# Performance work log

Hardware: AMD Instinct MI355X
Metric: run time of the kernel (lower is better)

The kernel has to match this reference:

```python
import jax, jax.numpy as jnp
import numpy as np

B, P, D_IN = 128, 4096, 4   # frames, points/frame, xyz+time
NG = 16                      # number of trajectory groups
H1, H2, H3 = 64, 128, 512    # PointNet shared-MLP widths


def _init_mlp(key, dims):
    ks = jax.random.split(key, len(dims) - 1)
    params = []
    for k, (di, do) in zip(ks, zip(dims[:-1], dims[1:])):
        W = jax.random.normal(k, (di, do), dtype=jnp.float32) * (1.0 / np.sqrt(di))
        b = jnp.zeros((do,), dtype=jnp.float32)
        params.append((W, b))
    return params


def setup_inputs() -> dict:
    key = jax.random.key(0)
    k_pc, k_t, k_idx, k_g, k_l = jax.random.split(key, 5)
    pc = jax.random.normal(k_pc, (B, 3, P), dtype=jnp.float32)
    traj_time_batch = jax.random.uniform(k_t, (B, 1), dtype=jnp.float32)
    traj_inbatch_index = jnp.sort(jax.random.randint(k_idx, (B,), 0, NG)).astype(jnp.int32)
    (Wg1, bg1), (Wg2, bg2), (Wg3, bg3) = _init_mlp(k_g, [D_IN, H1, H2, H3])
    (Wl1, bl1), (Wl2, bl2), (Wl3, bl3) = _init_mlp(k_l, [D_IN, H1, H2, H3])
    return dict(pc=pc, traj_time_batch=traj_time_batch, traj_inbatch_index=traj_inbatch_index,
                Wg1=Wg1, bg1=bg1, Wg2=Wg2, bg2=bg2, Wg3=Wg3, bg3=bg3,
                Wl1=Wl1, bl1=bl1, Wl2=Wl2, bl2=bl2, Wl3=Wl3, bl3=bl3)


def _mlp(x, layers):
    # pointwise shared MLP: x [..., P, d_in] -> [..., P, d_out]
    for W, b in layers:
        x = jax.nn.relu(x @ W + b)
    return x


def reference(pc, traj_time_batch, traj_inbatch_index,
              Wg1, bg1, Wg2, bg2, Wg3, bg3,
              Wl1, bl1, Wl2, bl2, Wl3, bl3):
    b, _, p = pc.shape
    # append time channel: [B,3,P] + [B,1,P] -> [B,4,P]
    t = jnp.broadcast_to(traj_time_batch[..., None], (b, 1, p))
    feat = jnp.concatenate([pc, t], axis=1)
    x = jnp.swapaxes(feat, 1, 2)  # [B,P,4] points-last layout for pointwise MLP

    # global branch: shared MLP on every point, then max over all points of each trajectory group
    hg = _mlp(x, [(Wg1, bg1), (Wg2, bg2), (Wg3, bg3)])           # [B,P,H3]
    seg = jnp.repeat(traj_inbatch_index, p)                       # [B*P]
    gmax = jax.ops.segment_max(hg.reshape(b * p, -1), seg, num_segments=NG)  # [NG,H3]
    global_feat = gmax[traj_inbatch_index]                        # [B,H3] broadcast back per frame

    # local branch: per-frame PointNet encode (shared MLP + max over points)
    hl = _mlp(x, [(Wl1, bl1), (Wl2, bl2), (Wl3, bl3)])            # [B,P,H3]
    local_feat = hl.max(axis=1)                                   # [B,H3]

    z = jnp.concatenate([global_feat, local_feat], axis=1)        # [B,2*H3]
    input_features_vis = pc                                       # original pc (last dim == 4096, no slice)
    return (z, input_features_vis)
```

## Files before the change

kernel.cpp:

```cpp
#include <hip/hip_runtime.h>
#include <hip/hip_bf16.h>

#define NB   128
#define NP   4096
#define NGRP 16
#define C3   512

typedef __bf16 bf16x8 __attribute__((ext_vector_type(8)));
typedef __bf16 bf16x4 __attribute__((ext_vector_type(4)));
typedef float  f32x4  __attribute__((ext_vector_type(4)));

#define WS_W1F_G 0
#define WS_W1F_L 4096
#define WS_W2F_G 8192
#define WS_W2F_L 24576
#define WS_W3F_G 40960
#define WS_W3F_L 172032
#define WS_GMAX  303104

__global__ __launch_bounds__(256) void prep_kernel(
    const float* __restrict__ Wg1, const float* __restrict__ Wg2, const float* __restrict__ Wg3,
    const float* __restrict__ Wl1, const float* __restrict__ Wl2, const float* __restrict__ Wl3,
    float* __restrict__ out, char* __restrict__ ws) {
    const int t = blockIdx.x, tid = threadIdx.x;
    if (t >= 37) {
        #pragma unroll
        for (int j = 0; j < 8; ++j) out[(t - 37) * 2048 + j * 256 + tid] = 0.0f;
        return;
    }
    if (t == 36) {
        float* gmax = (float*)(ws + WS_GMAX);
        #pragma unroll
        for (int k = 0; k < 32; ++k) gmax[k * 256 + tid] = 0.0f;
        int c = tid >> 6, lane = tid & 63;
        int ch = c * 16 + (lane & 15);
        int kb = (lane >> 4) * 8;
        bf16x8 pg, pl;
        #pragma unroll
        for (int j = 0; j < 8; ++j) {
            int k = kb + j;
            pg[j] = (k < 4) ? (__bf16)Wg1[k * 64 + ch] : (__bf16)0.0f;
            pl[j] = (k < 4) ? (__bf16)Wl1[k * 64 + ch] : (__bf16)0.0f;
        }
        *(bf16x8*)((__bf16*)(ws + WS_W1F_G) + c * 512 + lane * 8) = pg;
        *(bf16x8*)((__bf16*)(ws + WS_W1F_L) + c * 512 + lane * 8) = pl;
        return;
    }
    __shared__ float tile[64][65];
    const float* src; __bf16* dst; int cBase, mMul, srcStride;
    if (t < 32) {
        int branch = t >> 4, rem = t & 15;
        int tk = rem >> 3, tc = rem & 7;
        src = (branch ? Wl3 : Wg3) + (size_t)(tk * 64) * 512 + tc * 64;
        dst = (__bf16*)(ws + (branch ? WS_W3F_L : WS_W3F_G));
        cBase = tc * 16 + tk * 2; mMul = 4; srcStride = 512;
    } else {
        int u = t - 32; int branch = u >> 1, tc = u & 1;
        src = (branch ? Wl2 : Wg2) + tc * 64;
        dst = (__bf16*)(ws + (branch ? WS_W2F_L : WS_W2F_G));
        cBase = tc * 8; mMul = 2; srcStride = 128;
    }
    {
        int r0 = tid >> 6, cl = tid & 63;
        #pragma unroll
        for (int p = 0; p < 16; ++p)
            tile[p * 4 + r0][cl] = src[(size_t)(p * 4 + r0) * srcStride + cl];
    }
    __syncthreads();
    int lane = tid & 63, l15 = lane & 15, q = lane >> 4;
    #pragma unroll
    for (int cc = 0; cc < 2; ++cc) {
        int pair = (tid >> 6) * 2 + cc;
        int mi = pair >> 1, ks = pair & 1;
        bf16x8 pk;
        #pragma unroll
        for (int j = 0; j < 8; ++j) pk[j] = (__bf16)tile[ks * 32 + q * 8 + j][mi * 16 + l15];
        *(bf16x8*)(dst + (cBase + mi * mMul + ks) * 512 + lane * 8) = pk;
    }
}

__global__ __launch_bounds__(512, 2) void main_kernel(
    const float* __restrict__ pc, const float* __restrict__ tt, const int* __restrict__ idx,
    const float* __restrict__ bg1, const float* __restrict__ bg2, const float* __restrict__ bg3,
    const float* __restrict__ bl1, const float* __restrict__ bl2, const float* __restrict__ bl3,
    float* __restrict__ out, char* __restrict__ ws) {
    __shared__ __align__(16) char smem[41728];
    __bf16* h2f = (__bf16*)smem;
    __bf16* h1f = (__bf16*)(smem + 32768);
    float*  b1s = (float*)(smem + 40960);
    float*  b2s = (float*)(smem + 41216);

    const int tid = threadIdx.x, lane = tid & 63, wave = tid >> 6;
    const int quad = lane >> 4, l15 = lane & 15;
    const int branch = blockIdx.y;
    const int frame = blockIdx.x >> 2, p0 = (blockIdx.x & 3) * 1024;

    const float* pcx = pc + (size_t)frame * 3 * NP;

    if (branch == 0) {
        f32x4* pd = (f32x4*)(out + NB * 2 * C3 + (size_t)frame * 3 * NP + p0);
        const f32x4* ps = (const f32x4*)(pcx + p0);
        for (int i = tid; i < 768; i += 512) {
            int r = i >> 8, col = i & 255;
            pd[r * (NP / 4) + col] = ps[r * (NP / 4) + col];
        }
    }

    const __bf16* w1g = (const __bf16*)(ws + (branch ? WS_W1F_L : WS_W1F_G));
    const __bf16* w2g = (const __bf16*)(ws + (branch ? WS_W2F_L : WS_W2F_G));
    const __bf16* w3g = (const __bf16*)(ws + (branch ? WS_W3F_L : WS_W3F_G));
    const float* b1 = branch ? bl1 : bg1;
    const float* b2 = branch ? bl2 : bg2;
    const float* b3 = branch ? bl3 : bg3;

    if (tid < 64)  b1s[tid] = b1[tid];
    if (tid < 128) b2s[tid] = b2[tid];

    bf16x8 a1[4];
    #pragma unroll
    for (int mi = 0; mi < 4; ++mi) a1[mi] = *(const bf16x8*)(w1g + mi * 512 + lane * 8);
    bf16x8 a2[2];
    #pragma unroll
    for (int ks = 0; ks < 2; ++ks)
        a2[ks] = *(const bf16x8*)(w2g + (wave * 2 + ks) * 512 + lane * 8);
    bf16x8 aw[4][4];
    #pragma unroll
    for (int mi = 0; mi < 4; ++mi)
        #pragma unroll
        for (int ks = 0; ks < 4; ++ks)
            aw[mi][ks] = *(const bf16x8*)(w3g + ((wave * 4 + mi) * 4 + ks) * 512 + lane * 8);

    const float tval = tt[frame];
    const f32x4 zf = {0.0f, 0.0f, 0.0f, 0.0f};
    f32x4 runmax[4];
    #pragma unroll
    for (int mi = 0; mi < 4; ++mi) runmax[mi] = (f32x4){-1e30f, -1e30f, -1e30f, -1e30f};

    const bool l1wave = (wave < 4);
    const int pw = (wave & 3) * 16 + l15;
    const int kq2 = (wave * 2 + (quad >> 1)) & 3;
    const int s2  = wave >> 1;

    auto do_l1 = [&](float xx, float xy, float xz) {
        bf16x8 xb;
        #pragma unroll
        for (int j = 0; j < 8; ++j) xb[j] = (__bf16)0.0f;
        if (quad == 0) { xb[0] = (__bf16)xx; xb[1] = (__bf16)xy; xb[2] = (__bf16)xz; xb[3] = (__bf16)tval; }
        #pragma unroll
        for (int mi = 0; mi < 4; ++mi) {
            f32x4 c = __builtin_amdgcn_mfma_f32_16x16x32_bf16(a1[mi], xb, zf, 0, 0, 0);
            f32x4 bv = *(const f32x4*)(b1s + mi * 16 + quad * 4);
            bf16x4 pk;
            #pragma unroll
            for (int r = 0; r < 4; ++r) pk[r] = (__bf16)fmaxf(c[r] + bv[r], 0.0f);
            const int kq = (mi & 1) * 2 + (quad >> 1);
            *(bf16x4*)(h1f + ((wave & 3) * 2 + (mi >> 1)) * 512 + kq * 128 + l15 * 8 + (quad & 1) * 4) = pk;
        }
    };
    auto do_l2 = [&](__bf16* hbn) {
        #pragma unroll
        for (int ni = 0; ni < 4; ++ni) {
            bf16x8 q0 = *(const bf16x8*)(h1f + (ni * 2 + 0) * 512 + lane * 8);
            bf16x8 q1 = *(const bf16x8*)(h1f + (ni * 2 + 1) * 512 + lane * 8);
            f32x4 c = __builtin_amdgcn_mfma_f32_16x16x32_bf16(a2[0], q0, zf, 0, 0, 0);
            c = __builtin_amdgcn_mfma_f32_16x16x32_bf16(a2[1], q1, c, 0, 0, 0);
            f32x4 bv = *(const f32x4*)(b2s + wave * 16 + quad * 4);
            bf16x4 pk;
            #pragma unroll
            for (int r = 0; r < 4; ++r) pk[r] = (__bf16)fmaxf(c[r] + bv[r], 0.0f);
            *(bf16x4*)(hbn + (ni * 4 + s2) * 512 + kq2 * 128 + l15 * 8 + (quad & 1) * 4) = pk;
        }
    };
    auto p2_group = [&](const __bf16* hb, int ni) {
        bf16x8 bh[4];
        #pragma unroll
        for (int ks = 0; ks < 4; ++ks)
            bh[ks] = *(const bf16x8*)(hb + (ni * 4 + ks) * 512 + lane * 8);
        f32x4 acc[4];
        #pragma unroll
        for (int ks = 0; ks < 4; ++ks)
            #pragma unroll
            for (int mi = 0; mi < 4; ++mi)
                acc[mi] = __builtin_amdgcn_mfma_f32_16x16x32_bf16(
                    aw[mi][ks], bh[ks], ks ? acc[mi] : zf, 0, 0, 0);
        #pragma unroll
        for (int mi = 0; mi < 4; ++mi)
            #pragma unroll
            for (int r = 0; r < 4; ++r)
                runmax[mi][r] = fmaxf(runmax[mi][r], acc[mi][r]);
    };

    __syncthreads();

    if (l1wave) {
        float xx = pcx[p0 + pw], xy = pcx[NP + p0 + pw], xz = pcx[2 * NP + p0 + pw];
        do_l1(xx, xy, xz);
    }
    __syncthreads();
    do_l2(h2f);

    for (int m = 0; m < 16; ++m) {
        __syncthreads();
        const __bf16* hb = h2f + (m & 1) * 8192;
        __bf16* hbn = h2f + ((m + 1) & 1) * 8192;
        const bool more = (m < 15);
        float nx = 0.f, ny = 0.f, nz = 0.f;
        if (more && l1wave) {
            const int p = p0 + (m + 1) * 64 + pw;
            nx = pcx[p]; ny = pcx[NP + p]; nz = pcx[2 * NP + p];
        }
        p2_group(hb, 0);
        p2_group(hb, 1);
        if (more && l1wave) do_l1(nx, ny, nz);
        __syncthreads();
        p2_group(hb, 2);
        p2_group(hb, 3);
        if (more) do_l2(hbn);
    }

    const int g = idx[frame];
    float* gmax = (float*)(ws + WS_GMAX);
    unsigned* dst = (branch == 0) ? (unsigned*)(gmax + g * C3)
                                  : (unsigned*)(out + (size_t)frame * (2 * C3) + C3);
    #pragma unroll
    for (int mi = 0; mi < 4; ++mi) {
        f32x4 v = runmax[mi];
        #pragma unroll
        for (int d = 1; d < 16; d <<= 1) {
            #pragma unroll
            for (int r = 0; r < 4; ++r) v[r] = fmaxf(v[r], __shfl_xor(v[r], d));
        }
        if (l15 == 0) {
            #pragma unroll
            for (int r = 0; r < 4; ++r) {
                const int ch = wave * 64 + mi * 16 + quad * 4 + r;
                const float fv = fmaxf(v[r] + b3[ch], 0.0f);
                atomicMax(dst + ch, __float_as_uint(fv));
            }
        }
    }
}

__global__ void gather_kernel(const int* __restrict__ idx, const char* __restrict__ ws,
                              float* __restrict__ out) {
    int i = blockIdx.x * blockDim.x + threadIdx.x;
    int b = i >> 9, ch = i & 511;
    const float* gmax = (const float*)(ws + WS_GMAX);
    out[b * (2 * C3) + ch] = gmax[idx[b] * C3 + ch];
}

extern "C" void kernel_launch(void* const* d_in, const int* in_sizes, int n_in,
                              void* d_out, int out_size, void* d_ws, size_t ws_size,
                              hipStream_t stream) {
    const float* pc  = (const float*)d_in[0];
    const float* tt  = (const float*)d_in[1];
    const int*   idx = (const int*)d_in[2];
    const float* Wg1 = (const float*)d_in[3];  const float* bg1 = (const float*)d_in[4];
    const float* Wg2 = (const float*)d_in[5];  const float* bg2 = (const float*)d_in[6];
    const float* Wg3 = (const float*)d_in[7];  const float* bg3 = (const float*)d_in[8];
    const float* Wl1 = (const float*)d_in[9];  const float* bl1 = (const float*)d_in[10];
    const float* Wl2 = (const float*)d_in[11]; const float* bl2 = (const float*)d_in[12];
    const float* Wl3 = (const float*)d_in[13]; const float* bl3 = (const float*)d_in[14];
    float* out = (float*)d_out;
    char*  ws  = (char*)d_ws;

    prep_kernel<<<101, 256, 0, stream>>>(Wg1, Wg2, Wg3, Wl1, Wl2, Wl3, out, ws);
    main_kernel<<<dim3(512, 2), 512, 0, stream>>>(pc, tt, idx, bg1, bg2, bg3,
                                                  bl1, bl2, bl3, out, ws);
    gather_kernel<<<256, 256, 0, stream>>>(idx, ws, out);
}
```

Measured before the change: 226.4 us.

## Fuse weight prep and gather into a warp-specialized per-frame kernel

Launches one block per frame and branch, splitting the waves into producers and consumers. Four producer waves compute layers 1 and 2 into double-buffered shared memory, while four consumer waves run the layer-3 MFMAs and a running max over 512 channels. The separate weight-prep and gather kernels are removed: weights are converted to bf16 fragments straight from fp32 global memory, and a last-arriving-block counter does the per-group max and broadcast. This drops launch overhead and the atomics, but only half the waves do the dominant layer-3 work, there are 4x fewer blocks, and 128 registers of weight fragments plus 32 of running max under the (512, 2) launch bounds risks register spills.

```diff
diff --git a/kernel.cpp b/kernel.cpp
--- a/kernel.cpp
+++ b/kernel.cpp
@@ -3,112 +3,48 @@
 
 #define NB   128
 #define NP   4096
-#define NGRP 16
 #define C3   512
 
 typedef __bf16 bf16x8 __attribute__((ext_vector_type(8)));
 typedef __bf16 bf16x4 __attribute__((ext_vector_type(4)));
 typedef float  f32x4  __attribute__((ext_vector_type(4)));
 
-#define WS_W1F_G 0
-#define WS_W1F_L 4096
-#define WS_W2F_G 8192
-#define WS_W2F_L 24576
-#define WS_W3F_G 40960
-#define WS_W3F_L 172032
-#define WS_GMAX  303104
-
-__global__ __launch_bounds__(256) void prep_kernel(
-    const float* __restrict__ Wg1, const float* __restrict__ Wg2, const float* __restrict__ Wg3,
-    const float* __restrict__ Wl1, const float* __restrict__ Wl2, const float* __restrict__ Wl3,
-    float* __restrict__ out, char* __restrict__ ws) {
-    const int t = blockIdx.x, tid = threadIdx.x;
-    if (t >= 37) {
-        #pragma unroll
-        for (int j = 0; j < 8; ++j) out[(t - 37) * 2048 + j * 256 + tid] = 0.0f;
-        return;
-    }
-    if (t == 36) {
-        float* gmax = (float*)(ws + WS_GMAX);
-        #pragma unroll
-        for (int k = 0; k < 32; ++k) gmax[k * 256 + tid] = 0.0f;
-        int c = tid >> 6, lane = tid & 63;
-        int ch = c * 16 + (lane & 15);
-        int kb = (lane >> 4) * 8;
-        bf16x8 pg, pl;
-        #pragma unroll
-        for (int j = 0; j < 8; ++j) {
-            int k = kb + j;
-            pg[j] = (k < 4) ? (__bf16)Wg1[k * 64 + ch] : (__bf16)0.0f;
-            pl[j] = (k < 4) ? (__bf16)Wl1[k * 64 + ch] : (__bf16)0.0f;
-        }
-        *(bf16x8*)((__bf16*)(ws + WS_W1F_G) + c * 512 + lane * 8) = pg;
-        *(bf16x8*)((__bf16*)(ws + WS_W1F_L) + c * 512 + lane * 8) = pl;
-        return;
-    }
-    __shared__ float tile[64][65];
-    const float* src; __bf16* dst; int cBase, mMul, srcStride;
-    if (t < 32) {
-        int branch = t >> 4, rem = t & 15;
-        int tk = rem >> 3, tc = rem & 7;
-        src = (branch ? Wl3 : Wg3) + (size_t)(tk * 64) * 512 + tc * 64;
-        dst = (__bf16*)(ws + (branch ? WS_W3F_L : WS_W3F_G));
-        cBase = tc * 16 + tk * 2; mMul = 4; srcStride = 512;
-    } else {
-        int u = t - 32; int branch = u >> 1, tc = u & 1;
-        src = (branch ? Wl2 : Wg2) + tc * 64;
-        dst = (__bf16*)(ws + (branch ? WS_W2F_L : WS_W2F_G));
-        cBase = tc * 8; mMul = 2; srcStride = 128;
-    }
-    {
-        int r0 = tid >> 6, cl = tid & 63;
-        #pragma unroll
-        for (int p = 0; p < 16; ++p)
-            tile[p * 4 + r0][cl] = src[(size_t)(p * 4 + r0) * srcStride + cl];
-    }
-    __syncthreads();
-    int lane = tid & 63, l15 = lane & 15, q = lane >> 4;
-    #pragma unroll
-    for (int cc = 0; cc < 2; ++cc) {
-        int pair = (tid >> 6) * 2 + cc;
-        int mi = pair >> 1, ks = pair & 1;
-        bf16x8 pk;
-        #pragma unroll
-        for (int j = 0; j < 8; ++j) pk[j] = (__bf16)tile[ks * 32 + q * 8 + j][mi * 16 + l15];
-        *(bf16x8*)(dst + (cBase + mi * mMul + ks) * 512 + lane * 8) = pk;
-    }
-}
+#define WS_PART 0
+#define WS_CNT  262144
 
 __global__ __launch_bounds__(512, 2) void main_kernel(
     const float* __restrict__ pc, const float* __restrict__ tt, const int* __restrict__ idx,
-    const float* __restrict__ bg1, const float* __restrict__ bg2, const float* __restrict__ bg3,
-    const float* __restrict__ bl1, const float* __restrict__ bl2, const float* __restrict__ bl3,
+    const float* __restrict__ Wg1, const float* __restrict__ bg1,
+    const float* __restrict__ Wg2, const float* __restrict__ bg2,
+    const float* __restrict__ Wg3, const float* __restrict__ bg3,
+    const float* __restrict__ Wl1, const float* __restrict__ bl1,
+    const float* __restrict__ Wl2, const float* __restrict__ bl2,
+    const float* __restrict__ Wl3, const float* __restrict__ bl3,
     float* __restrict__ out, char* __restrict__ ws) {
-    __shared__ __align__(16) char smem[41728];
+    __shared__ __align__(16) char smem[49928];
     __bf16* h2f = (__bf16*)smem;
     __bf16* h1f = (__bf16*)(smem + 32768);
-    float*  b1s = (float*)(smem + 40960);
-    float*  b2s = (float*)(smem + 41216);
+    float*  b1s = (float*)(smem + 49152);
+    float*  b2s = (float*)(smem + 49408);
+    int*  sflag = (int*)(smem + 49920);
 
     const int tid = threadIdx.x, lane = tid & 63, wave = tid >> 6;
     const int quad = lane >> 4, l15 = lane & 15;
-    const int branch = blockIdx.y;
-    const int frame = blockIdx.x >> 2, p0 = (blockIdx.x & 3) * 1024;
+    const int branch = blockIdx.y, frame = blockIdx.x;
+    const bool prod = (wave < 4);
 
     const float* pcx = pc + (size_t)frame * 3 * NP;
 
     if (branch == 0) {
-        f32x4* pd = (f32x4*)(out + NB * 2 * C3 + (size_t)frame * 3 * NP + p0);
-        const f32x4* ps = (const f32x4*)(pcx + p0);
-        for (int i = tid; i < 768; i += 512) {
-            int r = i >> 8, col = i & 255;
-            pd[r * (NP / 4) + col] = ps[r * (NP / 4) + col];
-        }
-    }
-
-    const __bf16* w1g = (const __bf16*)(ws + (branch ? WS_W1F_L : WS_W1F_G));
-    const __bf16* w2g = (const __bf16*)(ws + (branch ? WS_W2F_L : WS_W2F_G));
-    const __bf16* w3g = (const __bf16*)(ws + (branch ? WS_W3F_L : WS_W3F_G));
+        const f32x4* ps = (const f32x4*)pcx;
+        f32x4* pd = (f32x4*)(out + NB * 2 * C3 + (size_t)frame * 3 * NP);
+        #pragma unroll
+        for (int j = 0; j < 6; ++j) pd[j * 512 + tid] = ps[j * 512 + tid];
+    }
+
+    const float* W1 = branch ? Wl1 : Wg1;
+    const float* W2 = branch ? Wl2 : Wg2;
+    const float* W3 = branch ? Wl3 : Wg3;
     const float* b1 = branch ? bl1 : bg1;
     const float* b2 = branch ? bl2 : bg2;
     const float* b3 = branch ? bl3 : bg3;
@@ -116,59 +52,81 @@
     if (tid < 64)  b1s[tid] = b1[tid];
     if (tid < 128) b2s[tid] = b2[tid];
 
-    bf16x8 a1[4];
-    #pragma unroll
-    for (int mi = 0; mi < 4; ++mi) a1[mi] = *(const bf16x8*)(w1g + mi * 512 + lane * 8);
-    bf16x8 a2[2];
-    #pragma unroll
-    for (int ks = 0; ks < 2; ++ks)
-        a2[ks] = *(const bf16x8*)(w2g + (wave * 2 + ks) * 512 + lane * 8);
-    bf16x8 aw[4][4];
-    #pragma unroll
-    for (int mi = 0; mi < 4; ++mi)
-        #pragma unroll
-        for (int ks = 0; ks < 4; ++ks)
-            aw[mi][ks] = *(const bf16x8*)(w3g + ((wave * 4 + mi) * 4 + ks) * 512 + lane * 8);
+    bf16x8 afr[8][4];
+    if (prod) {
+        #pragma unroll
+        for (int mi = 0; mi < 4; ++mi) {
+            bf16x8 f;
+            #pragma unroll
+            for (int j = 0; j < 8; ++j)
+                f[j] = (quad == 0 && j < 4) ? (__bf16)W1[j * 64 + mi * 16 + l15] : (__bf16)0.0f;
+            afr[0][mi] = f;
+        }
+        #pragma unroll
+        for (int mi = 0; mi < 2; ++mi)
+            #pragma unroll
+            for (int ks = 0; ks < 2; ++ks) {
+                bf16x8 f;
+                #pragma unroll
+                for (int j = 0; j < 8; ++j)
+                    f[j] = (__bf16)W2[(ks * 32 + quad * 8 + j) * 128 + wave * 32 + mi * 16 + l15];
+                afr[1][mi * 2 + ks] = f;
+            }
+    } else {
+        const int cb = (wave - 4) * 128;
+        #pragma unroll
+        for (int mi = 0; mi < 8; ++mi)
+            #pragma unroll
+            for (int ks = 0; ks < 4; ++ks) {
+                bf16x8 f;
+                #pragma unroll
+                for (int j = 0; j < 8; ++j)
+                    f[j] = (__bf16)W3[(ks * 32 + quad * 8 + j) * 512 + cb + mi * 16 + l15];
+                afr[mi][ks] = f;
+            }
+    }
 
     const float tval = tt[frame];
     const f32x4 zf = {0.0f, 0.0f, 0.0f, 0.0f};
-    f32x4 runmax[4];
+    f32x4 runmax[8];
     #pragma unroll
-    for (int mi = 0; mi < 4; ++mi) runmax[mi] = (f32x4){-1e30f, -1e30f, -1e30f, -1e30f};
-
-    const bool l1wave = (wave < 4);
-    const int pw = (wave & 3) * 16 + l15;
-    const int kq2 = (wave * 2 + (quad >> 1)) & 3;
-    const int s2  = wave >> 1;
-
-    auto do_l1 = [&](float xx, float xy, float xz) {
+    for (int mi = 0; mi < 8; ++mi) runmax[mi] = (f32x4){-1e30f, -1e30f, -1e30f, -1e30f};
+
+    const int pw = wave * 16 + l15;
+
+    auto do_l1 = [&](int m, __bf16* dst) {
+        const int p = m * 64 + pw;
+        const float xx = pcx[p], xy = pcx[NP + p], xz = pcx[2 * NP + p];
         bf16x8 xb;
         #pragma unroll
         for (int j = 0; j < 8; ++j) xb[j] = (__bf16)0.0f;
         if (quad == 0) { xb[0] = (__bf16)xx; xb[1] = (__bf16)xy; xb[2] = (__bf16)xz; xb[3] = (__bf16)tval; }
         #pragma unroll
         for (int mi = 0; mi < 4; ++mi) {
-            f32x4 c = __builtin_amdgcn_mfma_f32_16x16x32_bf16(a1[mi], xb, zf, 0, 0, 0);
+            f32x4 c = __builtin_amdgcn_mfma_f32_16x16x32_bf16(afr[0][mi], xb, zf, 0, 0, 0);
             f32x4 bv = *(const f32x4*)(b1s + mi * 16 + quad * 4);
             bf16x4 pk;
             #pragma unroll
             for (int r = 0; r < 4; ++r) pk[r] = (__bf16)fmaxf(c[r] + bv[r], 0.0f);
             const int kq = (mi & 1) * 2 + (quad >> 1);
-            *(bf16x4*)(h1f + ((wave & 3) * 2 + (mi >> 1)) * 512 + kq * 128 + l15 * 8 + (quad & 1) * 4) = pk;
+            *(bf16x4*)(dst + (wave * 2 + (mi >> 1)) * 512 + kq * 128 + l15 * 8 + (quad & 1) * 4) = pk;
         }
     };
-    auto do_l2 = [&](__bf16* hbn) {
+    auto do_l2 = [&](const __bf16* src, __bf16* dst) {
         #pragma unroll
         for (int ni = 0; ni < 4; ++ni) {
-            bf16x8 q0 = *(const bf16x8*)(h1f + (ni * 2 + 0) * 512 + lane * 8);
-            bf16x8 q1 = *(const bf16x8*)(h1f + (ni * 2 + 1) * 512 + lane * 8);
-            f32x4 c = __builtin_amdgcn_mfma_f32_16x16x32_bf16(a2[0], q0, zf, 0, 0, 0);
-            c = __builtin_amdgcn_mfma_f32_16x16x32_bf16(a2[1], q1, c, 0, 0, 0);
-            f32x4 bv = *(const f32x4*)(b2s + wave * 16 + quad * 4);
-            bf16x4 pk;
-            #pragma unroll
-            for (int r = 0; r < 4; ++r) pk[r] = (__bf16)fmaxf(c[r] + bv[r], 0.0f);
-            *(bf16x4*)(hbn + (ni * 4 + s2) * 512 + kq2 * 128 + l15 * 8 + (quad & 1) * 4) = pk;
+            bf16x8 q0 = *(const bf16x8*)(src + (ni * 2 + 0) * 512 + lane * 8);
+            bf16x8 q1 = *(const bf16x8*)(src + (ni * 2 + 1) * 512 + lane * 8);
+            #pragma unroll
+            for (int mi = 0; mi < 2; ++mi) {
+                f32x4 c = __builtin_amdgcn_mfma_f32_16x16x32_bf16(afr[1][mi * 2 + 0], q0, zf, 0, 0, 0);
+                c = __builtin_amdgcn_mfma_f32_16x16x32_bf16(afr[1][mi * 2 + 1], q1, c, 0, 0, 0);
+                f32x4 bv = *(const f32x4*)(b2s + wave * 32 + mi * 16 + quad * 4);
+                bf16x4 pk;
+                #pragma unroll
+                for (int r = 0; r < 4; ++r) pk[r] = (__bf16)fmaxf(c[r] + bv[r], 0.0f);
+                *(bf16x4*)(dst + (ni * 4 + wave) * 512 + (mi * 2 + (quad >> 1)) * 128 + l15 * 8 + (quad & 1) * 4) = pk;
+            }
         }
     };
     auto p2_group = [&](const __bf16* hb, int ni) {
@@ -176,77 +134,83 @@
         #pragma unroll
         for (int ks = 0; ks < 4; ++ks)
             bh[ks] = *(const bf16x8*)(hb + (ni * 4 + ks) * 512 + lane * 8);
-        f32x4 acc[4];
-        #pragma unroll
-        for (int ks = 0; ks < 4; ++ks)
-            #pragma unroll
-            for (int mi = 0; mi < 4; ++mi)
-                acc[mi] = __builtin_amdgcn_mfma_f32_16x16x32_bf16(
-                    aw[mi][ks], bh[ks], ks ? acc[mi] : zf, 0, 0, 0);
-        #pragma unroll
-        for (int mi = 0; mi < 4; ++mi)
-            #pragma unroll
-            for (int r = 0; r < 4; ++r)
-                runmax[mi][r] = fmaxf(runmax[mi][r], acc[mi][r]);
+        #pragma unroll
+        for (int half = 0; half < 2; ++half) {
+            f32x4 acc[4];
+            #pragma unroll
+            for (int ks = 0; ks < 4; ++ks)
+                #pragma unroll
+                for (int m2 = 0; m2 < 4; ++m2)
+                    acc[m2] = __builtin_amdgcn_mfma_f32_16x16x32_bf16(
+                        afr[half * 4 + m2][ks], bh[ks], ks ? acc[m2] : zf, 0, 0, 0);
+            #pragma unroll
+            for (int m2 = 0; m2 < 4; ++m2)
+                #pragma unroll
+                for (int r = 0; r < 4; ++r)
+                    runmax[half * 4 + m2][r] = fmaxf(runmax[half * 4 + m2][r], acc[m2][r]);
+        }
     };
 
     __syncthreads();
-
-    if (l1wave) {
-        float xx = pcx[p0 + pw], xy = pcx[NP + p0 + pw], xz = pcx[2 * NP + p0 + pw];
-        do_l1(xx, xy, xz);
-    }
+    if (prod) do_l1(0, h1f);
     __syncthreads();
-    do_l2(h2f);
-
-    for (int m = 0; m < 16; ++m) {
-        __syncthreads();
+    if (prod) { do_l2(h1f, h2f); do_l1(1, h1f + 4096); }
+    __syncthreads();
+
+    for (int m = 0; m < 64; ++m) {
         const __bf16* hb = h2f + (m & 1) * 8192;
         __bf16* hbn = h2f + ((m + 1) & 1) * 8192;
-        const bool more = (m < 15);
-        float nx = 0.f, ny = 0.f, nz = 0.f;
-        if (more && l1wave) {
-            const int p = p0 + (m + 1) * 64 + pw;
-            nx = pcx[p]; ny = pcx[NP + p]; nz = pcx[2 * NP + p];
-        }
-        p2_group(hb, 0);
-        p2_group(hb, 1);
-        if (more && l1wave) do_l1(nx, ny, nz);
-        __syncthreads();
-        p2_group(hb, 2);
-        p2_group(hb, 3);
-        if (more) do_l2(hbn);
-    }
-
-    const int g = idx[frame];
-    float* gmax = (float*)(ws + WS_GMAX);
-    unsigned* dst = (branch == 0) ? (unsigned*)(gmax + g * C3)
-                                  : (unsigned*)(out + (size_t)frame * (2 * C3) + C3);
-    #pragma unroll
-    for (int mi = 0; mi < 4; ++mi) {
-        f32x4 v = runmax[mi];
-        #pragma unroll
-        for (int d = 1; d < 16; d <<= 1) {
-            #pragma unroll
-            for (int r = 0; r < 4; ++r) v[r] = fmaxf(v[r], __shfl_xor(v[r], d));
-        }
-        if (l15 == 0) {
-            #pragma unroll
-            for (int r = 0; r < 4; ++r) {
-                const int ch = wave * 64 + mi * 16 + quad * 4 + r;
-                const float fv = fmaxf(v[r] + b3[ch], 0.0f);
-                atomicMax(dst + ch, __float_as_uint(fv));
-            }
-        }
-    }
-}
-
-__global__ void gather_kernel(const int* __restrict__ idx, const char* __restrict__ ws,
-                              float* __restrict__ out) {
-    int i = blockIdx.x * blockDim.x + threadIdx.x;
-    int b = i >> 9, ch = i & 511;
-    const float* gmax = (const float*)(ws + WS_GMAX);
-    out[b * (2 * C3) + ch] = gmax[idx[b] * C3 + ch];
+        if (!prod) { p2_group(hb, 0); p2_group(hb, 1); }
+        else if (m < 63) do_l2(h1f + ((m + 1) & 1) * 4096, hbn);
+        __syncthreads();
+        if (!prod) { p2_group(hb, 2); p2_group(hb, 3); }
+        else if (m < 62) do_l1(m + 2, h1f + (m & 1) * 4096);
+        __syncthreads();
+    }
+
+    float* partial = (float*)(ws + WS_PART);
+    if (!prod) {
+        const int cb = (wave - 4) * 128;
+        #pragma unroll
+        for (int mi = 0; mi < 8; ++mi) {
+            f32x4 v = runmax[mi];
+            #pragma unroll
+            for (int d = 1; d < 16; d <<= 1) {
+                #pragma unroll
+                for (int r = 0; r < 4; ++r) v[r] = fmaxf(v[r], __shfl_xor(v[r], d));
+            }
+            if (l15 == 0) {
+                #pragma unroll
+                for (int r = 0; r < 4; ++r) {
+                    const int ch = cb + mi * 16 + quad * 4 + r;
+                    const float fv = fmaxf(v[r] + b3[ch], 0.0f);
+                    if (branch) out[(size_t)frame * (2 * C3) + C3 + ch] = fv;
+                    else        partial[frame * C3 + ch] = fv;
+                }
+            }
+        }
+    }
+
+    if (branch == 0) {
+        const int g = idx[frame];
+        __threadfence();
+        __syncthreads();
+        if (tid == 0) {
+            int gs = 0;
+            for (int f2 = 0; f2 < NB; ++f2) gs += (idx[f2] == g);
+            int old = atomicAdd((int*)(ws + WS_CNT) + g, 1);
+            *sflag = (old == gs - 1);
+        }
+        __syncthreads();
+        if (*sflag) {
+            __threadfence();
+            float mx = 0.0f;
+            for (int f2 = 0; f2 < NB; ++f2)
+                if (idx[f2] == g) mx = fmaxf(mx, partial[f2 * C3 + tid]);
+            for (int f2 = 0; f2 < NB; ++f2)
+                if (idx[f2] == g) out[(size_t)f2 * (2 * C3) + tid] = mx;
+        }
+    }
 }
 
 extern "C" void kernel_launch(void* const* d_in, const int* in_sizes, int n_in,
@@ -264,8 +228,8 @@
     float* out = (float*)d_out;
     char*  ws  = (char*)d_ws;
 
-    prep_kernel<<<101, 256, 0, stream>>>(Wg1, Wg2, Wg3, Wl1, Wl2, Wl3, out, ws);
-    main_kernel<<<dim3(512, 2), 512, 0, stream>>>(pc, tt, idx, bg1, bg2, bg3,
-                                                  bl1, bl2, bl3, out, ws);
-    gather_kernel<<<256, 256, 0, stream>>>(idx, ws, out);
+    hipMemsetAsync(ws + WS_CNT, 0, 16 * sizeof(int), stream);
+    main_kernel<<<dim3(128, 2), 512, 0, stream>>>(
+        pc, tt, idx, Wg1, bg1, Wg2, bg2, Wg3, bg3,
+        Wl1, bl1, Wl2, bl2, Wl3, bl3, out, ws);
 }
```

Result: slower. 249.9 us (+10.4%).
